# Kernel optimization log

Hardware: AMD Instinct MI355X
Metric: run time of the kernel (lower is better)

## Reference

```python
import jax, jax.numpy as jnp
import numpy as np

WINDOW_SIZE = 7
SIGMA = 1.5


def _gaussian_window(size, sigma, channel):
    coords = jnp.arange(size, dtype=jnp.float32) - size // 2
    g = jnp.exp(-coords ** 2 / (2.0 * sigma ** 2))
    g = g / g.sum()
    g3d = g[:, None, None] * g[None, :, None] * g[None, None, :]  # [k,k,k]
    # depthwise kernel: [out_ch=channel, in_ch/groups=1, kD, kH, kW]
    return jnp.broadcast_to(g3d[None, None], (channel, 1, size, size, size))


def _depthwise_conv3d(x, window):
    ch = x.shape[1]
    return jax.lax.conv_general_dilated(
        x, window,
        window_strides=(1, 1, 1),
        padding='SAME',
        dimension_numbers=('NCDHW', 'OIDHW', 'NCDHW'),
        feature_group_count=ch,
    )


def setup_inputs() -> dict:
    key = jax.random.key(0)
    k1, k2 = jax.random.split(key)
    shape = (4, 1, 160, 160, 160)
    prediction = jax.random.uniform(k1, shape, dtype=jnp.float32)
    target = jax.random.uniform(k2, shape, dtype=jnp.float32)
    return {"prediction": prediction, "target": target}


def reference(prediction, target):
    C1 = 0.01 ** 2
    C2 = 0.03 ** 2
    ch = prediction.shape[1]
    window = _gaussian_window(WINDOW_SIZE, SIGMA, ch).astype(prediction.dtype)

    mu_pred = _depthwise_conv3d(prediction, window)
    mu_tgt = _depthwise_conv3d(target, window)
    mu_pred_sq = mu_pred ** 2
    mu_tgt_sq = mu_tgt ** 2
    mu_cross = mu_pred * mu_tgt

    sigma_pred_sq = _depthwise_conv3d(prediction ** 2, window) - mu_pred_sq
    sigma_tgt_sq = _depthwise_conv3d(target ** 2, window) - mu_tgt_sq
    sigma_cross = _depthwise_conv3d(prediction * target, window) - mu_cross

    ssim_map = ((2.0 * mu_cross + C1) * (2.0 * sigma_cross + C2)) / (
        (mu_pred_sq + mu_tgt_sq + C1) * (sigma_pred_sq + sigma_tgt_sq + C2))
    return 1.0 - ssim_map.mean()
```

## Files before the change

### kernel.cpp

```cpp
#include <hip/hip_runtime.h>
#include <hip/hip_fp16.h>

#define DIM   160
#define DIM2  25600
#define TY    32
#define TX    32
#define TZ    16
#define HY    38
#define HX    38
#define SS    51
#define YSTR  39
#define YCH   (TY * YSTR)
#define NSL   22
#define NSITE (HY * HX)
#define NVOX_D 16384000.0

#define W0 0.03663285f
#define W1 0.11128076f
#define W2 0.21674532f
#define W3 0.27068213f

__global__ void ssim_zero_acc(double* acc) {
    if (threadIdx.x == 0 && blockIdx.x == 0) acc[0] = 0.0;
}

__global__ __launch_bounds__(256, 3) void ssim_main(const float* __restrict__ P,
                                                    const float* __restrict__ T,
                                                    double* __restrict__ acc) {
    const float Wf[7] = {W0, W1, W2, W3, W2, W1, W0};
    const __half2 wh[7] = {__float2half2_rn(W0), __float2half2_rn(W1),
                           __float2half2_rn(W2), __float2half2_rn(W3),
                           __float2half2_rn(W2), __float2half2_rn(W1),
                           __float2half2_rn(W0)};

    __shared__ __half2 sIn[HY * SS];
    __shared__ __half2 ycMu[YCH];
    __shared__ __half2 ycE2[YCH];
    __shared__ float   ycPt[YCH];
    __shared__ float   red[4];

    const int tid = threadIdx.x;
    int bid = blockIdx.x;
    int b  = bid / 250;  int r  = bid - b * 250;
    int zc = r / 25;     int r2 = r - zc * 25;
    int ty = r2 / 5;     int tx = r2 - ty * 5;

    const int base = b * (DIM * DIM * DIM);
    const int z0 = zc * TZ, y0 = ty * TY - 3, x0 = tx * TX - 3;

    int gofs[6], lofs[6];
    bool ld[6], st[6];
#pragma unroll
    for (int k = 0; k < 6; ++k) {
        int u = tid + 256 * k;
        st[k] = (u < NSITE);
        int y = u / HX, x = u - y * HX;
        int gy = y0 + y, gx = x0 + x;
        ld[k] = st[k] & ((unsigned)gy < (unsigned)DIM) & ((unsigned)gx < (unsigned)DIM);
        gofs[k] = gy * DIM + gx;
        lofs[k] = y * SS + x;
    }

    int ybR[3], ybW[3];
#pragma unroll
    for (int q = 0; q < 3; ++q) {
        int t = tid + 256 * q; if (t > 607) t = 607;
        int yy = t / HX, x = t - yy * HX;
        ybR[q] = (2 * yy) * SS + x;
        ybW[q] = (2 * yy) * YSTR + x;
    }

    const int xrd = (tid >> 3) * YSTR + 4 * (tid & 7);

    const __half2 hz = __float2half2_rn(0.f);
    __half2 azMu[4][7], azE2[4][7], azPtA[7], azPtB[7];
#pragma unroll
    for (int o = 0; o < 4; ++o)
#pragma unroll
        for (int j = 0; j < 7; ++j) { azMu[o][j] = hz; azE2[o][j] = hz; }
#pragma unroll
    for (int j = 0; j < 7; ++j) { azPtA[j] = hz; azPtB[j] = hz; }

    float lsum = 0.f;

    auto ytask = [&](int rb, int wb) {
        __half2 mu0 = hz, mu1 = hz, e20 = hz, e21 = hz;
        float pt0 = 0.f, pt1 = 0.f;
#pragma unroll
        for (int k = 0; k < 8; ++k) {
            __half2 v  = sIn[rb + k * SS];
            __half2 v2 = __hmul2(v, v);
            __half2 vs = __halves2half2(__high2half(v), __low2half(v));
            float ptf  = __low2float(__hmul2(v, vs));
            if (k < 7) {
                mu0 = __hfma2(wh[k], v, mu0);
                e20 = __hfma2(wh[k], v2, e20);
                pt0 = fmaf(Wf[k], ptf, pt0);
            }
            if (k >= 1) {
                mu1 = __hfma2(wh[k - 1], v, mu1);
                e21 = __hfma2(wh[k - 1], v2, e21);
                pt1 = fmaf(Wf[k - 1], ptf, pt1);
            }
        }
        ycMu[wb] = mu0; ycMu[wb + YSTR] = mu1;
        ycE2[wb] = e20; ycE2[wb + YSTR] = e21;
        ycPt[wb] = pt0; ycPt[wb + YSTR] = pt1;
    };

    {
        int zs = z0 - 3;
        bool zok = (unsigned)zs < (unsigned)DIM;
        const float* Pp = P + base + zs * DIM2;
        const float* Tp = T + base + zs * DIM2;
        float rp[6], rt[6];
#pragma unroll
        for (int k = 0; k < 6; ++k) {
            rp[k] = 0.f; rt[k] = 0.f;
            if (zok && ld[k]) { rp[k] = Pp[gofs[k]]; rt[k] = Tp[gofs[k]]; }
        }
#pragma unroll
        for (int k = 0; k < 6; ++k)
            if (st[k]) sIn[lofs[k]] = __floats2half2_rn(rp[k], rt[k]);
    }
    __syncthreads();

    for (int i = 0; i < NSL; ++i) {
        const bool hn = (i + 1 < NSL);
        float rp[6], rt[6];

        if (hn) {
            int zs = z0 + i - 2;
            bool zok = (unsigned)zs < (unsigned)DIM;
            const float* Pp = P + base + zs * DIM2;
            const float* Tp = T + base + zs * DIM2;
#pragma unroll
            for (int k = 0; k < 6; ++k) {
                rp[k] = 0.f; rt[k] = 0.f;
                if (zok && ld[k]) { rp[k] = Pp[gofs[k]]; rt[k] = Tp[gofs[k]]; }
            }
        }

        ytask(ybR[0], ybW[0]);
        ytask(ybR[1], ybW[1]);
        if (tid < 96) ytask(ybR[2], ybW[2]);
        __syncthreads();

        __half2 muw[10], e2w[10]; float ptw[10];
#pragma unroll
        for (int m = 0; m < 10; ++m) {
            muw[m] = ycMu[xrd + m];
            e2w[m] = ycE2[xrd + m];
            ptw[m] = ycPt[xrd + m];
        }
        __half2 xmu[4], xe2[4]; float xpt[4];
#pragma unroll
        for (int o = 0; o < 4; ++o) {
            __half2 am = hz, ae = hz; float ap = 0.f;
#pragma unroll
            for (int k = 0; k < 7; ++k) {
                am = __hfma2(wh[k], muw[o + k], am);
                ae = __hfma2(wh[k], e2w[o + k], ae);
                ap = fmaf(Wf[k], ptw[o + k], ap);
            }
            xmu[o] = am; xe2[o] = ae; xpt[o] = ap;
        }

        __half2 ptA = __floats2half2_rn(xpt[0], xpt[1]);
        __half2 ptB = __floats2half2_rn(xpt[2], xpt[3]);
#pragma unroll
        for (int j = 0; j < 7; ++j) {
            __half2 w2 = wh[6 - j];
#pragma unroll
            for (int o = 0; o < 4; ++o) {
                azMu[o][j] = __hfma2(w2, xmu[o], azMu[o][j]);
                azE2[o][j] = __hfma2(w2, xe2[o], azE2[o][j]);
            }
            azPtA[j] = __hfma2(w2, ptA, azPtA[j]);
            azPtB[j] = __hfma2(w2, ptB, azPtB[j]);
        }

        if (i >= 6) {
            float eptv[4] = {__low2float(azPtA[0]), __high2float(azPtA[0]),
                             __low2float(azPtB[0]), __high2float(azPtB[0])};
#pragma unroll
            for (int o = 0; o < 4; ++o) {
                float mp = __low2float(azMu[o][0]), mt = __high2float(azMu[o][0]);
                float ep2 = __low2float(azE2[o][0]), et2 = __high2float(azE2[o][0]);
                float mp2 = mp * mp, mt2 = mt * mt, mpt = mp * mt;
                float num = fmaf(2.f, mpt, 1e-4f) * fmaf(2.f, eptv[o] - mpt, 9e-4f);
                float den = (mp2 + mt2 + 1e-4f) * ((ep2 - mp2) + (et2 - mt2) + 9e-4f);
                lsum += num * __builtin_amdgcn_rcpf(den);
            }
        }

#pragma unroll
        for (int j = 0; j < 6; ++j) {
#pragma unroll
            for (int o = 0; o < 4; ++o) {
                azMu[o][j] = azMu[o][j + 1];
                azE2[o][j] = azE2[o][j + 1];
            }
            azPtA[j] = azPtA[j + 1];
            azPtB[j] = azPtB[j + 1];
        }
#pragma unroll
        for (int o = 0; o < 4; ++o) { azMu[o][6] = hz; azE2[o][6] = hz; }
        azPtA[6] = hz; azPtB[6] = hz;

        if (hn) {
#pragma unroll
            for (int k = 0; k < 6; ++k)
                if (st[k]) sIn[lofs[k]] = __floats2half2_rn(rp[k], rt[k]);
        }
        __syncthreads();
    }

#pragma unroll
    for (int off = 32; off > 0; off >>= 1) lsum += __shfl_down(lsum, off);
    if ((tid & 63) == 0) red[tid >> 6] = lsum;
    __syncthreads();
    if (tid == 0) atomicAdd(acc, (double)(red[0] + red[1] + red[2] + red[3]));
}

__global__ void ssim_finalize(const double* __restrict__ acc, float* __restrict__ out) {
    if (threadIdx.x == 0 && blockIdx.x == 0)
        out[0] = 1.f - (float)(acc[0] / NVOX_D);
}

extern "C" void kernel_launch(void* const* d_in, const int* in_sizes, int n_in,
                              void* d_out, int out_size, void* d_ws, size_t ws_size,
                              hipStream_t stream) {
    const float* P = (const float*)d_in[0];
    const float* T = (const float*)d_in[1];
    float* out = (float*)d_out;
    double* acc = (double*)d_ws;

    ssim_zero_acc<<<1, 64, 0, stream>>>(acc);
    ssim_main<<<4 * 10 * 5 * 5, 256, 0, stream>>>(P, T, acc);
    ssim_finalize<<<1, 64, 0, stream>>>(acc, out);
}
```

Before: 103.2 us.

## Shrink tile to 16x32 with 20-deep z and two outputs per thread

```diff
diff --git a/kernel.cpp b/kernel.cpp
--- a/kernel.cpp
+++ b/kernel.cpp
@@ -3,15 +3,14 @@
 
 #define DIM   160
 #define DIM2  25600
-#define TY    32
+#define TY    16
 #define TX    32
-#define TZ    16
-#define HY    38
+#define TZ    20
+#define HY    22
 #define HX    38
 #define SS    51
 #define YSTR  39
-#define YCH   (TY * YSTR)
-#define NSL   22
+#define NSL   26
 #define NSITE (HY * HX)
 #define NVOX_D 16384000.0
 
@@ -24,7 +23,7 @@
     if (threadIdx.x == 0 && blockIdx.x == 0) acc[0] = 0.0;
 }
 
-__global__ __launch_bounds__(256, 3) void ssim_main(const float* __restrict__ P,
+__global__ __launch_bounds__(256, 4) void ssim_main(const float* __restrict__ P,
                                                     const float* __restrict__ T,
                                                     double* __restrict__ acc) {
     const float Wf[7] = {W0, W1, W2, W3, W2, W1, W0};
@@ -34,24 +33,24 @@
                            __float2half2_rn(W0)};
 
     __shared__ __half2 sIn[HY * SS];
-    __shared__ __half2 ycMu[YCH];
-    __shared__ __half2 ycE2[YCH];
-    __shared__ float   ycPt[YCH];
+    __shared__ __half2 ycMu[TY * YSTR];
+    __shared__ __half2 ycE2[TY * YSTR];
+    __shared__ float   ycPt[TY * YSTR];
     __shared__ float   red[4];
 
     const int tid = threadIdx.x;
     int bid = blockIdx.x;
-    int b  = bid / 250;  int r  = bid - b * 250;
-    int zc = r / 25;     int r2 = r - zc * 25;
+    int b  = bid / 400;  int r  = bid - b * 400;
+    int zc = r / 50;     int r2 = r - zc * 50;
     int ty = r2 / 5;     int tx = r2 - ty * 5;
 
     const int base = b * (DIM * DIM * DIM);
     const int z0 = zc * TZ, y0 = ty * TY - 3, x0 = tx * TX - 3;
 
-    int gofs[6], lofs[6];
-    bool ld[6], st[6];
-#pragma unroll
-    for (int k = 0; k < 6; ++k) {
+    int gofs[4], lofs[4];
+    bool ld[4], st[4];
+#pragma unroll
+    for (int k = 0; k < 4; ++k) {
         int u = tid + 256 * k;
         st[k] = (u < NSITE);
         int y = u / HX, x = u - y * HX;
@@ -61,25 +60,28 @@
         lofs[k] = y * SS + x;
     }
 
-    int ybR[3], ybW[3];
-#pragma unroll
-    for (int q = 0; q < 3; ++q) {
-        int t = tid + 256 * q; if (t > 607) t = 607;
+    int ybR0, ybW0, ybR1, ybW1;
+    {
+        int t = tid;
         int yy = t / HX, x = t - yy * HX;
-        ybR[q] = (2 * yy) * SS + x;
-        ybW[q] = (2 * yy) * YSTR + x;
-    }
-
-    const int xrd = (tid >> 3) * YSTR + 4 * (tid & 7);
+        ybR0 = (2 * yy) * SS + x;
+        ybW0 = (2 * yy) * YSTR + x;
+        int t1 = tid + 256; if (t1 > 303) t1 = 303;
+        int yy1 = t1 / HX, x1 = t1 - yy1 * HX;
+        ybR1 = (2 * yy1) * SS + x1;
+        ybW1 = (2 * yy1) * YSTR + x1;
+    }
+
+    const int xrd = (tid >> 4) * YSTR + 2 * (tid & 15);
 
     const __half2 hz = __float2half2_rn(0.f);
-    __half2 azMu[4][7], azE2[4][7], azPtA[7], azPtB[7];
-#pragma unroll
-    for (int o = 0; o < 4; ++o)
+    __half2 azMu[2][7], azE2[2][7], azPt[7];
+#pragma unroll
+    for (int o = 0; o < 2; ++o)
 #pragma unroll
         for (int j = 0; j < 7; ++j) { azMu[o][j] = hz; azE2[o][j] = hz; }
 #pragma unroll
-    for (int j = 0; j < 7; ++j) { azPtA[j] = hz; azPtB[j] = hz; }
+    for (int j = 0; j < 7; ++j) azPt[j] = hz;
 
     float lsum = 0.f;
 
@@ -113,21 +115,21 @@
         bool zok = (unsigned)zs < (unsigned)DIM;
         const float* Pp = P + base + zs * DIM2;
         const float* Tp = T + base + zs * DIM2;
-        float rp[6], rt[6];
-#pragma unroll
-        for (int k = 0; k < 6; ++k) {
+        float rp[4], rt[4];
+#pragma unroll
+        for (int k = 0; k < 4; ++k) {
             rp[k] = 0.f; rt[k] = 0.f;
             if (zok && ld[k]) { rp[k] = Pp[gofs[k]]; rt[k] = Tp[gofs[k]]; }
         }
 #pragma unroll
-        for (int k = 0; k < 6; ++k)
+        for (int k = 0; k < 4; ++k)
             if (st[k]) sIn[lofs[k]] = __floats2half2_rn(rp[k], rt[k]);
     }
     __syncthreads();
 
     for (int i = 0; i < NSL; ++i) {
         const bool hn = (i + 1 < NSL);
-        float rp[6], rt[6];
+        float rp[4], rt[4];
 
         if (hn) {
             int zs = z0 + i - 2;
@@ -135,27 +137,26 @@
             const float* Pp = P + base + zs * DIM2;
             const float* Tp = T + base + zs * DIM2;
 #pragma unroll
-            for (int k = 0; k < 6; ++k) {
+            for (int k = 0; k < 4; ++k) {
                 rp[k] = 0.f; rt[k] = 0.f;
                 if (zok && ld[k]) { rp[k] = Pp[gofs[k]]; rt[k] = Tp[gofs[k]]; }
             }
         }
 
-        ytask(ybR[0], ybW[0]);
-        ytask(ybR[1], ybW[1]);
-        if (tid < 96) ytask(ybR[2], ybW[2]);
+        ytask(ybR0, ybW0);
+        if (tid < 48) ytask(ybR1, ybW1);
         __syncthreads();
 
-        __half2 muw[10], e2w[10]; float ptw[10];
-#pragma unroll
-        for (int m = 0; m < 10; ++m) {
+        __half2 muw[8], e2w[8]; float ptw[8];
+#pragma unroll
+        for (int m = 0; m < 8; ++m) {
             muw[m] = ycMu[xrd + m];
             e2w[m] = ycE2[xrd + m];
             ptw[m] = ycPt[xrd + m];
         }
-        __half2 xmu[4], xe2[4]; float xpt[4];
-#pragma unroll
-        for (int o = 0; o < 4; ++o) {
+        __half2 xmu[2], xe2[2]; float xpt[2];
+#pragma unroll
+        for (int o = 0; o < 2; ++o) {
             __half2 am = hz, ae = hz; float ap = 0.f;
 #pragma unroll
             for (int k = 0; k < 7; ++k) {
@@ -166,25 +167,21 @@
             xmu[o] = am; xe2[o] = ae; xpt[o] = ap;
         }
 
-        __half2 ptA = __floats2half2_rn(xpt[0], xpt[1]);
-        __half2 ptB = __floats2half2_rn(xpt[2], xpt[3]);
+        __half2 ptp = __floats2half2_rn(xpt[0], xpt[1]);
 #pragma unroll
         for (int j = 0; j < 7; ++j) {
             __half2 w2 = wh[6 - j];
-#pragma unroll
-            for (int o = 0; o < 4; ++o) {
-                azMu[o][j] = __hfma2(w2, xmu[o], azMu[o][j]);
-                azE2[o][j] = __hfma2(w2, xe2[o], azE2[o][j]);
-            }
-            azPtA[j] = __hfma2(w2, ptA, azPtA[j]);
-            azPtB[j] = __hfma2(w2, ptB, azPtB[j]);
+            azMu[0][j] = __hfma2(w2, xmu[0], azMu[0][j]);
+            azMu[1][j] = __hfma2(w2, xmu[1], azMu[1][j]);
+            azE2[0][j] = __hfma2(w2, xe2[0], azE2[0][j]);
+            azE2[1][j] = __hfma2(w2, xe2[1], azE2[1][j]);
+            azPt[j]    = __hfma2(w2, ptp,    azPt[j]);
         }
 
         if (i >= 6) {
-            float eptv[4] = {__low2float(azPtA[0]), __high2float(azPtA[0]),
-                             __low2float(azPtB[0]), __high2float(azPtB[0])};
-#pragma unroll
-            for (int o = 0; o < 4; ++o) {
+            float eptv[2] = {__low2float(azPt[0]), __high2float(azPt[0])};
+#pragma unroll
+            for (int o = 0; o < 2; ++o) {
                 float mp = __low2float(azMu[o][0]), mt = __high2float(azMu[o][0]);
                 float ep2 = __low2float(azE2[o][0]), et2 = __high2float(azE2[o][0]);
                 float mp2 = mp * mp, mt2 = mt * mt, mpt = mp * mt;
@@ -196,21 +193,19 @@
 
 #pragma unroll
         for (int j = 0; j < 6; ++j) {
-#pragma unroll
-            for (int o = 0; o < 4; ++o) {
-                azMu[o][j] = azMu[o][j + 1];
-                azE2[o][j] = azE2[o][j + 1];
-            }
-            azPtA[j] = azPtA[j + 1];
-            azPtB[j] = azPtB[j + 1];
-        }
-#pragma unroll
-        for (int o = 0; o < 4; ++o) { azMu[o][6] = hz; azE2[o][6] = hz; }
-        azPtA[6] = hz; azPtB[6] = hz;
+            azMu[0][j] = azMu[0][j + 1];
+            azMu[1][j] = azMu[1][j + 1];
+            azE2[0][j] = azE2[0][j + 1];
+            azE2[1][j] = azE2[1][j + 1];
+            azPt[j]    = azPt[j + 1];
+        }
+        azMu[0][6] = hz; azMu[1][6] = hz;
+        azE2[0][6] = hz; azE2[1][6] = hz;
+        azPt[6] = hz;
 
         if (hn) {
 #pragma unroll
-            for (int k = 0; k < 6; ++k)
+            for (int k = 0; k < 4; ++k)
                 if (st[k]) sIn[lofs[k]] = __floats2half2_rn(rp[k], rt[k]);
         }
         __syncthreads();
@@ -237,6 +232,6 @@
     double* acc = (double*)d_ws;
 
     ssim_zero_acc<<<1, 64, 0, stream>>>(acc);
-    ssim_main<<<4 * 10 * 5 * 5, 256, 0, stream>>>(P, T, acc);
+    ssim_main<<<4 * 8 * 10 * 5, 256, 0, stream>>>(P, T, acc);
     ssim_finalize<<<1, 64, 0, stream>>>(acc, out);
 }
```

After: 111.4 us. 8.0% more time.
